# Kernel optimization log

Hardware: AMD Instinct MI355X
Metric: run time of the kernel (lower is better)

Reference implementation:

```python
import jax, jax.numpy as jnp
import numpy as np
from jax import lax

EPS_COS = 1e-8  # torch F.cosine_similarity eps
EPS_GN = 1e-5   # torch GroupNorm eps


def setup_inputs() -> dict:
    key = jax.random.key(0)
    k1, k2, k3 = jax.random.split(key, 3)
    b, f, h, w = 4, 64, 64, 64
    fdm = jax.random.uniform(k1, (b, 1, 2 * h, 2 * w), dtype=jnp.float32)
    x = jax.random.normal(k2, (b, f, h, w), dtype=jnp.float32)
    W_fuse = jax.random.normal(k3, (f, 2 * f, 3, 3), dtype=jnp.float32) * 0.05
    b_fuse = jnp.zeros((f,), jnp.float32)
    gamma = jnp.ones((f,), jnp.float32)
    beta = jnp.zeros((f,), jnp.float32)
    return {"fdm": fdm, "x": x, "W_fuse": W_fuse, "b_fuse": b_fuse,
            "gamma": gamma, "beta": beta}


def reference(fdm, x, W_fuse, b_fuse, gamma, beta):
    b, f, h, w = x.shape
    # adaptive_max_pool2d(fdm, (h, w)): input spatial is exact multiple -> plain max pool
    kh, kw = fdm.shape[2] // h, fdm.shape[3] // w
    fdm_p = lax.reduce_window(fdm, -jnp.inf, lax.max,
                              (1, 1, kh, kw), (1, 1, kh, kw), 'VALID')  # [b,1,h,w]
    # per-sample threshold: min(0.5, max(fdm)/3)
    maxv = jnp.max(fdm_p, axis=(1, 2, 3))                 # [b]
    thre = jnp.minimum(0.5, maxv / 3.0)                   # [b]
    mask = fdm_p.reshape(b, h * w) >= thre[:, None]       # [b, HW] selected pixels

    # cosine similarity between selected feature vectors and all positions.
    # Original masked-selects N rows then computes N x HW sims and max-reduces over N;
    # we compute the full HW x HW sim and mask unselected rows to -inf (same max).
    xf = x.reshape(b, f, h * w).transpose(0, 2, 1)        # [b, HW, f]
    norm = jnp.sqrt(jnp.sum(xf * xf, axis=-1, keepdims=True))
    xn = xf / jnp.maximum(norm, EPS_COS)
    sim = jnp.einsum('bpf,bqf->bpq', xn, xn)              # [b, HW(sel), HW(all)]
    sim = jnp.where(mask[:, :, None], sim, -jnp.inf)
    sm = (jnp.max(sim, axis=1) / 2.0 + 0.5).reshape(b, 1, h, w)

    # fuse: Conv2d(2f -> f, k3, pad1) + GroupNorm(1, f) + ReLU
    cat = jnp.concatenate([sm * x, x], axis=1)            # [b, 2f, h, w]
    y = lax.conv_general_dilated(cat, W_fuse, (1, 1), 'SAME',
                                 dimension_numbers=('NCHW', 'OIHW', 'NCHW'))
    y = y + b_fuse[None, :, None, None]
    mu = jnp.mean(y, axis=(1, 2, 3), keepdims=True)
    var = jnp.mean((y - mu) ** 2, axis=(1, 2, 3), keepdims=True)
    y = (y - mu) / jnp.sqrt(var + EPS_GN)
    y = y * gamma[None, :, None, None] + beta[None, :, None, None]
    x0 = jax.nn.relu(y)
    return x0, sm
```

## Files before the change

kernel.cpp:

```cpp
#include <hip/hip_runtime.h>
#include <math.h>


#define HW 4096
#define NCH 64

typedef __attribute__((ext_vector_type(8))) short short8;
typedef __attribute__((ext_vector_type(4))) float f32x4;

static __device__ __forceinline__ ushort f2bf(float f) {
    unsigned u = __float_as_uint(f);
    unsigned r = (u + 0x7fffu + ((u >> 16) & 1u)) >> 16;
    return (ushort)r;
}
static __device__ __forceinline__ float bf2f(ushort h) {
    return __uint_as_float(((unsigned)h) << 16);
}
static __device__ __forceinline__ unsigned mapf(float f) {
    unsigned u = __float_as_uint(f);
    return u ^ ((unsigned)((int)u >> 31) | 0x80000000u);
}
static __device__ __forceinline__ float unmapf(unsigned u) {
    unsigned b = (u & 0x80000000u) ? (u ^ 0x80000000u) : ~u;
    return __uint_as_float(b);
}

__global__ __launch_bounds__(256) void k_pnp(
    const float* __restrict__ fdm, const float* __restrict__ x, const float* __restrict__ W,
    float* __restrict__ pooledOut, float* __restrict__ threOut,
    int* __restrict__ unsel, int* __restrict__ unselN, unsigned* __restrict__ scores,
    float* __restrict__ gnS1, float* __restrict__ gnS2,
    float* __restrict__ rn, float* __restrict__ smOut, ushort* __restrict__ inb,
    ushort* __restrict__ wbh, ushort* __restrict__ wbl) {
    const int t = threadIdx.x;
    if (blockIdx.x < 4) {
        const int b = blockIdx.x;
        __shared__ float pooled[4096];
        __shared__ float red[256];
        __shared__ int cnt;
        const float* fb = fdm + b * 16384;
        float lmax = -1.0f;
#pragma unroll
        for (int it = 0; it < 8; ++it) {
            int id2 = it * 256 + t;
            int i = id2 >> 5;
            int j2 = id2 & 31;
            const float* base = fb + i * 256 + j2 * 4;
            float4 a = *(const float4*)base;
            float4 c = *(const float4*)(base + 128);
            float p0 = fmaxf(fmaxf(a.x, a.y), fmaxf(c.x, c.y));
            float p1 = fmaxf(fmaxf(a.z, a.w), fmaxf(c.z, c.w));
            pooled[i * 64 + j2 * 2]     = p0;
            pooled[i * 64 + j2 * 2 + 1] = p1;
            lmax = fmaxf(lmax, fmaxf(p0, p1));
        }
        red[t] = lmax;
        __syncthreads();
        for (int s = 128; s > 0; s >>= 1) {
            if (t < s) red[t] = fmaxf(red[t], red[t + s]);
            __syncthreads();
        }
        __shared__ float thre_s;
        if (t == 0) {
            thre_s = fminf(0.5f, red[0] / 3.0f);
            cnt = 0;
            gnS1[b] = 0.0f; gnS2[b] = 0.0f;
        }
        __syncthreads();
        const float th = thre_s;
#pragma unroll
        for (int it = 0; it < 4; ++it) {
            int idx = (it * 256 + t) * 4;
            *(float4*)(pooledOut + b * 4096 + idx) = *(const float4*)(pooled + idx);
        }
        for (int idx = t; idx < 4096; idx += 256) {
            scores[b * 4096 + idx] = 0u;
            if (!(pooled[idx] >= th)) {
                int pos = atomicAdd(&cnt, 1);
                unsel[b * 4096 + pos] = idx;
            }
        }
        __syncthreads();
        if (t == 0) { unselN[b] = cnt; threOut[b] = th; }
    } else if (blockIdx.x < 260) {
        __shared__ float s_part[4][64];
        const int n = blockIdx.x - 4;
        const int b = n >> 6;
        const int pbase = (n & 63) * 64;
        const int wv = t >> 6;
        const int l = t & 63;
        const int sp = pbase + l;
        const float* xp = x + b * (NCH * HW) + sp;
        float xv[16];
        float ss = 0.f;
#pragma unroll
        for (int i = 0; i < 16; ++i) {
            float a = xp[(wv * 16 + i) * HW];
            xv[i] = a;
            ss += a * a;
        }
        s_part[wv][l] = ss;
        ushort h[16];
#pragma unroll
        for (int i = 0; i < 16; ++i) h[i] = f2bf(xv[i]);
        size_t dst1 = ((size_t)(b * 8 + wv) * 4096 + sp) * 16;
        size_t dst2 = ((size_t)(b * 8 + 4 + wv) * 4096 + sp) * 16;
        *(uint4*)(inb + dst1)     = *(const uint4*)h;
        *(uint4*)(inb + dst1 + 8) = *(const uint4*)(h + 8);
        *(uint4*)(inb + dst2)     = *(const uint4*)h;
        *(uint4*)(inb + dst2 + 8) = *(const uint4*)(h + 8);
        __syncthreads();
        if (t < 64) {
            float s = s_part[0][l] + s_part[1][l] + s_part[2][l] + s_part[3][l];
            int g = b * HW + pbase + l;
            rn[g] = 1.0f / fmaxf(sqrtf(s), 1e-8f);
            smOut[g] = 1.0f;
        }
    } else {
        const int u = (blockIdx.x - 260) * 256 + t;
        const int tap = u >> 10;
        const int rem = u & 1023;
        const int oc = rem >> 4;
        const int g = rem & 15;
        ushort hh[8], ll[8];
#pragma unroll
        for (int j = 0; j < 8; ++j) {
            int ic = g * 8 + j;
            float v = W[(oc * 128 + ic) * 9 + tap];
            ushort hb = f2bf(v);
            hh[j] = hb;
            ll[j] = f2bf(v - bf2f(hb));
        }
        *(uint4*)(wbh + (size_t)u * 8) = *(const uint4*)hh;
        *(uint4*)(wbl + (size_t)u * 8) = *(const uint4*)ll;
    }
}

__global__ __launch_bounds__(256) void k_score(
    const float* __restrict__ x, const float* __restrict__ rn,
    const float* __restrict__ pooledM, const float* __restrict__ threArr,
    const int* __restrict__ unsel, const int* __restrict__ unselN,
    const ushort* __restrict__ inb, unsigned* __restrict__ scores) {
    const int b = blockIdx.y;
    const int n0 = blockIdx.x * 128;
    const int t = threadIdx.x;
    const int lane = t & 63;
    const int wave = t >> 6;
    const int li = lane & 15;
    const int quad = lane >> 4;
    const int nu = unselN[b];
    if (nu == 0) return;

    __shared__ __align__(16) ushort s_qh[64 * 72];
    __shared__ __align__(16) ushort s_ql[64 * 72];
    __shared__ unsigned s_best[64];

    const float th = threArr[b];
    const int p0 = n0 + (2 * wave) * 16 + li;
    const int p1 = n0 + (2 * wave + 1) * 16 + li;
    const float rp0 = rn[b * 4096 + p0];
    const float rp1 = rn[b * 4096 + p1];
    const float ng0 = (pooledM[b * 4096 + p0] >= th) ? 0.0f : -INFINITY;
    const float ng1 = (pooledM[b * 4096 + p1] >= th) ? 0.0f : -INFINITY;

    for (int qs0 = 0; qs0 < nu; qs0 += 64) {
        __syncthreads();
        for (int idx = t; idx < 4096; idx += 256) {
            int q_l = idx >> 6;
            int c = idx & 63;
            int qg = qs0 + q_l;
            float v = 0.0f;
            if (qg < nu) {
                int q = unsel[b * 4096 + qg];
                v = x[b * (NCH * HW) + c * HW + q] * rn[b * 4096 + q];
            }
            ushort hb = f2bf(v);
            s_qh[q_l * 72 + c] = hb;
            s_ql[q_l * 72 + c] = f2bf(v - bf2f(hb));
        }
        if (t < 64) s_best[t] = 0u;
        __syncthreads();

        f32x4 acc[2][4];
#pragma unroll
        for (int nt = 0; nt < 2; ++nt)
#pragma unroll
            for (int mt = 0; mt < 4; ++mt) acc[nt][mt] = (f32x4){0.f, 0.f, 0.f, 0.f};
#pragma unroll
        for (int k0 = 0; k0 < 2; ++k0) {
            const int cb = k0 * 32 + quad * 8;
            const int grp = 4 + (cb >> 4);
            const int sub = cb & 15;
            short8 b0 = *(const short8*)(inb + (((size_t)(b * 8 + grp) * 4096) + p0) * 16 + sub);
            short8 b1 = *(const short8*)(inb + (((size_t)(b * 8 + grp) * 4096) + p1) * 16 + sub);
#pragma unroll
            for (int mt = 0; mt < 4; ++mt) {
                short8 ah = *(const short8*)(s_qh + (size_t)(mt * 16 + li) * 72 + cb);
                short8 al = *(const short8*)(s_ql + (size_t)(mt * 16 + li) * 72 + cb);
                acc[0][mt] = __builtin_amdgcn_mfma_f32_16x16x32_bf16(ah, b0, acc[0][mt], 0, 0, 0);
                acc[0][mt] = __builtin_amdgcn_mfma_f32_16x16x32_bf16(al, b0, acc[0][mt], 0, 0, 0);
                acc[1][mt] = __builtin_amdgcn_mfma_f32_16x16x32_bf16(ah, b1, acc[1][mt], 0, 0, 0);
                acc[1][mt] = __builtin_amdgcn_mfma_f32_16x16x32_bf16(al, b1, acc[1][mt], 0, 0, 0);
            }
        }
#pragma unroll
        for (int mt = 0; mt < 4; ++mt) {
#pragma unroll
            for (int r = 0; r < 4; ++r) {
                float sc = fmaxf(acc[0][mt][r] * rp0 + ng0, acc[1][mt][r] * rp1 + ng1);
                sc = fmaxf(sc, __shfl_xor(sc, 1));
                sc = fmaxf(sc, __shfl_xor(sc, 2));
                sc = fmaxf(sc, __shfl_xor(sc, 4));
                sc = fmaxf(sc, __shfl_xor(sc, 8));
                if (li == 0) atomicMax(&s_best[mt * 16 + quad * 4 + r], mapf(sc));
            }
        }
        __syncthreads();
        if (t < 64 && qs0 + t < nu) atomicMax(scores + b * 4096 + qs0 + t, s_best[t]);
    }
}

__global__ __launch_bounds__(256) void k_conv_mfma(
    const ushort* __restrict__ inb, const ushort* __restrict__ wbh, const ushort* __restrict__ wbl,
    const float* __restrict__ bfuse, const int* __restrict__ unsel, const int* __restrict__ unselN,
    const unsigned* __restrict__ scores, float* __restrict__ smOut,
    float* __restrict__ y, float* __restrict__ gnS1, float* __restrict__ gnS2) {
    const int rowblk = blockIdx.x;
    const int ocblk = blockIdx.y;
    const int b = blockIdx.z;
    const int t = threadIdx.x;
    const int lane = t & 63;
    const int wave = t >> 6;
    const int li = lane & 15;
    const int quad = lane >> 4;
    const int h0 = rowblk * 4;
    const int oc0 = ocblk * 16;
    const int nu = unselN[b];

    __shared__ __align__(16) ushort s_in[6 * 66 * 40];
    __shared__ __align__(16) ushort s_wh[9 * 16 * 40];
    __shared__ __align__(16) ushort s_wl[9 * 16 * 40];
    __shared__ float red1[256];
    __shared__ float red2[256];

    if (rowblk == 0 && ocblk == 0) {
        for (int qi = t; qi < nu; qi += 256) {
            float sm = unmapf(scores[b * 4096 + qi]) * 0.5f + 0.5f;
            smOut[b * 4096 + unsel[b * 4096 + qi]] = sm;
        }
    }

    f32x4 acc[4];
#pragma unroll
    for (int j = 0; j < 4; ++j) acc[j] = (f32x4){0.f, 0.f, 0.f, 0.f};

    for (int chunk = 0; chunk < 4; ++chunk) {
        __syncthreads();
        for (int idx = t; idx < 1584; idx += 256) {
            int part = idx & 3;
            int cell = idx >> 2;
            int r = cell / 66;
            int c = cell - r * 66;
            int h = h0 + r - 1;
            int w = c - 1;
            uint4 v = make_uint4(0u, 0u, 0u, 0u);
            if ((unsigned)h < 64u && (unsigned)w < 64u) {
                int grp = 2 * chunk + (part >> 1);
                int sub = part & 1;
                v = *(const uint4*)(inb + (((size_t)(b * 8 + grp) * 4096 + h * 64 + w) * 16 + sub * 8));
            }
            *(uint4*)(s_in + (size_t)cell * 40 + part * 8) = v;
        }
        const int ic0 = chunk * 32;
        for (int idx = t; idx < 1152; idx += 256) {
            int part = idx & 3;
            int uu = idx >> 2;
            int hl = uu / 144;
            int rem = uu - hl * 144;
            int tap = rem >> 4;
            int o = rem & 15;
            const ushort* src = (hl ? wbl : wbh) + ((size_t)(tap * 64 + oc0 + o) * 128 + ic0 + part * 8);
            uint4 v = *(const uint4*)src;
            ushort* dst = (hl ? s_wl : s_wh) + ((size_t)(tap * 16 + o) * 40 + part * 8);
            *(uint4*)dst = v;
        }
        if (chunk < 2) {
            __syncthreads();
            for (int idx = t; idx < nu * 4; idx += 256) {
                int qi = idx >> 2;
                int part = idx & 3;
                int q = unsel[b * 4096 + qi];
                int hq = q >> 6, wq = q & 63;
                int r = hq - h0 + 1;
                if ((unsigned)r < 6u) {
                    float sm = unmapf(scores[b * 4096 + qi]) * 0.5f + 0.5f;
                    ushort* ptr = s_in + (size_t)(r * 66 + wq + 1) * 40 + part * 8;
                    ushort hv[8];
                    *(uint4*)hv = *(const uint4*)ptr;
#pragma unroll
                    for (int j = 0; j < 8; ++j) hv[j] = f2bf(bf2f(hv[j]) * sm);
                    *(uint4*)ptr = *(const uint4*)hv;
                }
            }
        }
        __syncthreads();
#pragma unroll
        for (int kh = 0; kh < 3; ++kh) {
            const int r = wave + kh;
#pragma unroll
            for (int kw = 0; kw < 3; ++kw) {
                const int tap = kh * 3 + kw;
                short8 ah = *(const short8*)(s_wh + (size_t)(tap * 16 + li) * 40 + quad * 8);
                short8 al = *(const short8*)(s_wl + (size_t)(tap * 16 + li) * 40 + quad * 8);
#pragma unroll
                for (int j = 0; j < 4; ++j) {
                    int c = j * 16 + li + kw;
                    short8 bv = *(const short8*)(s_in + ((size_t)(r * 66 + c) * 40 + quad * 8));
                    acc[j] = __builtin_amdgcn_mfma_f32_16x16x32_bf16(ah, bv, acc[j], 0, 0, 0);
                    acc[j] = __builtin_amdgcn_mfma_f32_16x16x32_bf16(al, bv, acc[j], 0, 0, 0);
                }
            }
        }
    }
    float bias[4];
#pragma unroll
    for (int reg = 0; reg < 4; ++reg) bias[reg] = bfuse[oc0 + quad * 4 + reg];
    float s1 = 0.f, s2 = 0.f;
    const int hrow = h0 + wave;
#pragma unroll
    for (int j = 0; j < 4; ++j) {
#pragma unroll
        for (int reg = 0; reg < 4; ++reg) {
            float v = acc[j][reg] + bias[reg];
            y[((size_t)(b * 64 + oc0 + quad * 4 + reg)) * HW + hrow * 64 + j * 16 + li] = v;
            s1 += v; s2 += v * v;
        }
    }
    red1[t] = s1; red2[t] = s2;
    __syncthreads();
    for (int s = 128; s > 0; s >>= 1) {
        if (t < s) { red1[t] += red1[t + s]; red2[t] += red2[t + s]; }
        __syncthreads();
    }
    if (t == 0) {
        atomicAdd(&gnS1[b], red1[0]);
        atomicAdd(&gnS2[b], red2[0]);
    }
}

__global__ void k_gn(float* __restrict__ out, const float* __restrict__ gnS1, const float* __restrict__ gnS2,
                     const float* __restrict__ gamma, const float* __restrict__ beta) {
    const int e = (blockIdx.x * 256 + threadIdx.x) * 4;
    const int b = e >> 18;
    const int c = (e >> 12) & 63;
    const float inv = 1.0f / 262144.0f;
    float mu = gnS1[b] * inv;
    float var = gnS2[b] * inv - mu * mu;
    float rs = rsqrtf(var + 1e-5f);
    float scale = rs * gamma[c];
    float shift = beta[c] - mu * scale;
    float4 v = *(const float4*)(out + e);
    float4 o;
    o.x = fmaxf(v.x * scale + shift, 0.0f);
    o.y = fmaxf(v.y * scale + shift, 0.0f);
    o.z = fmaxf(v.z * scale + shift, 0.0f);
    o.w = fmaxf(v.w * scale + shift, 0.0f);
    *(float4*)(out + e) = o;
}

extern "C" void kernel_launch(void* const* d_in, const int* in_sizes, int n_in,
                              void* d_out, int out_size, void* d_ws, size_t ws_size,
                              hipStream_t stream) {
    const float* fdm   = (const float*)d_in[0];
    const float* x     = (const float*)d_in[1];
    const float* Wf    = (const float*)d_in[2];
    const float* bfuse = (const float*)d_in[3];
    const float* gamma = (const float*)d_in[4];
    const float* beta  = (const float*)d_in[5];
    float* out = (float*)d_out;
    float* ws  = (float*)d_ws;

    float*    rn      = ws;
    float*    pooledM = rn + 16384;
    int*      unsel   = (int*)(pooledM + 16384);
    unsigned* scores  = (unsigned*)(unsel + 16384);
    float*    thre    = (float*)(scores + 16384);
    int*      unselN  = (int*)(thre + 4);
    float*    gnS1    = (float*)(unselN + 4);
    float*    gnS2    = gnS1 + 4;
    ushort*   wbh     = (ushort*)(gnS2 + 4);
    ushort*   wbl     = wbh + 73728;
    ushort*   inb     = wbl + 73728;

    float* yout  = out;
    float* smOut = out + 1048576;

    k_pnp<<<dim3(296), dim3(256), 0, stream>>>(fdm, x, Wf, pooledM, thre, unsel, unselN,
                                               scores, gnS1, gnS2, rn, smOut, inb, wbh, wbl);
    k_score<<<dim3(32, 4), dim3(256), 0, stream>>>(x, rn, pooledM, thre, unsel, unselN, inb, scores);
    k_conv_mfma<<<dim3(16, 4, 4), dim3(256), 0, stream>>>(inb, wbh, wbl, bfuse, unsel, unselN,
                                                          scores, smOut, yout, gnS1, gnS2);
    k_gn<<<dim3(1024), dim3(256), 0, stream>>>(yout, gnS1, gnS2, gamma, beta);
}
```

Before: 114.4 us.

## Store bf16 input once, gather scores from it, prefetch conv chunks in registers

Measured after the change: 120.5 us. +5.3%, slower.

```diff
diff --git a/kernel.cpp b/kernel.cpp
--- a/kernel.cpp
+++ b/kernel.cpp
@@ -103,12 +103,9 @@
         ushort h[16];
 #pragma unroll
         for (int i = 0; i < 16; ++i) h[i] = f2bf(xv[i]);
-        size_t dst1 = ((size_t)(b * 8 + wv) * 4096 + sp) * 16;
-        size_t dst2 = ((size_t)(b * 8 + 4 + wv) * 4096 + sp) * 16;
-        *(uint4*)(inb + dst1)     = *(const uint4*)h;
-        *(uint4*)(inb + dst1 + 8) = *(const uint4*)(h + 8);
-        *(uint4*)(inb + dst2)     = *(const uint4*)h;
-        *(uint4*)(inb + dst2 + 8) = *(const uint4*)(h + 8);
+        size_t dst = ((size_t)(b * 4 + wv) * 4096 + sp) * 16;
+        *(uint4*)(inb + dst)     = *(const uint4*)h;
+        *(uint4*)(inb + dst + 8) = *(const uint4*)(h + 8);
         __syncthreads();
         if (t < 64) {
             float s = s_part[0][l] + s_part[1][l] + s_part[2][l] + s_part[3][l];
@@ -137,12 +134,11 @@
 }
 
 __global__ __launch_bounds__(256) void k_score(
-    const float* __restrict__ x, const float* __restrict__ rn,
-    const float* __restrict__ pooledM, const float* __restrict__ threArr,
+    const float* __restrict__ rn, const float* __restrict__ pooledM, const float* __restrict__ threArr,
     const int* __restrict__ unsel, const int* __restrict__ unselN,
     const ushort* __restrict__ inb, unsigned* __restrict__ scores) {
     const int b = blockIdx.y;
-    const int n0 = blockIdx.x * 128;
+    const int n0 = blockIdx.x * 64;
     const int t = threadIdx.x;
     const int lane = t & 63;
     const int wave = t >> 6;
@@ -156,58 +152,60 @@
     __shared__ unsigned s_best[64];
 
     const float th = threArr[b];
-    const int p0 = n0 + (2 * wave) * 16 + li;
-    const int p1 = n0 + (2 * wave + 1) * 16 + li;
+    const int p0 = n0 + wave * 16 + li;
     const float rp0 = rn[b * 4096 + p0];
-    const float rp1 = rn[b * 4096 + p1];
     const float ng0 = (pooledM[b * 4096 + p0] >= th) ? 0.0f : -INFINITY;
-    const float ng1 = (pooledM[b * 4096 + p1] >= th) ? 0.0f : -INFINITY;
 
     for (int qs0 = 0; qs0 < nu; qs0 += 64) {
         __syncthreads();
-        for (int idx = t; idx < 4096; idx += 256) {
-            int q_l = idx >> 6;
-            int c = idx & 63;
+        for (int idx = t; idx < 512; idx += 256) {
+            int q_l = idx >> 3;
+            int part = idx & 7;
             int qg = qs0 + q_l;
-            float v = 0.0f;
+            int q = 0;
+            float rq = 0.0f;
             if (qg < nu) {
-                int q = unsel[b * 4096 + qg];
-                v = x[b * (NCH * HW) + c * HW + q] * rn[b * 4096 + q];
-            }
-            ushort hb = f2bf(v);
-            s_qh[q_l * 72 + c] = hb;
-            s_ql[q_l * 72 + c] = f2bf(v - bf2f(hb));
+                q = unsel[b * 4096 + qg];
+                rq = rn[b * 4096 + q];
+            }
+            uint4 raw = *(const uint4*)(inb + (((size_t)(b * 4 + (part >> 1)) * 4096) + q) * 16 + (part & 1) * 8);
+            ushort hv[8]; *(uint4*)hv = raw;
+            ushort hh[8], ll[8];
+#pragma unroll
+            for (int j = 0; j < 8; ++j) {
+                float v = bf2f(hv[j]) * rq;
+                hh[j] = f2bf(v);
+                ll[j] = f2bf(v - bf2f(hh[j]));
+            }
+            int c0 = (part >> 1) * 16 + (part & 1) * 8;
+            *(uint4*)(s_qh + q_l * 72 + c0) = *(const uint4*)hh;
+            *(uint4*)(s_ql + q_l * 72 + c0) = *(const uint4*)ll;
         }
         if (t < 64) s_best[t] = 0u;
         __syncthreads();
 
-        f32x4 acc[2][4];
-#pragma unroll
-        for (int nt = 0; nt < 2; ++nt)
-#pragma unroll
-            for (int mt = 0; mt < 4; ++mt) acc[nt][mt] = (f32x4){0.f, 0.f, 0.f, 0.f};
+        f32x4 acc[4];
+#pragma unroll
+        for (int mt = 0; mt < 4; ++mt) acc[mt] = (f32x4){0.f, 0.f, 0.f, 0.f};
 #pragma unroll
         for (int k0 = 0; k0 < 2; ++k0) {
             const int cb = k0 * 32 + quad * 8;
-            const int grp = 4 + (cb >> 4);
+            const int grp = cb >> 4;
             const int sub = cb & 15;
-            short8 b0 = *(const short8*)(inb + (((size_t)(b * 8 + grp) * 4096) + p0) * 16 + sub);
-            short8 b1 = *(const short8*)(inb + (((size_t)(b * 8 + grp) * 4096) + p1) * 16 + sub);
+            short8 b0 = *(const short8*)(inb + (((size_t)(b * 4 + grp) * 4096) + p0) * 16 + sub);
 #pragma unroll
             for (int mt = 0; mt < 4; ++mt) {
                 short8 ah = *(const short8*)(s_qh + (size_t)(mt * 16 + li) * 72 + cb);
                 short8 al = *(const short8*)(s_ql + (size_t)(mt * 16 + li) * 72 + cb);
-                acc[0][mt] = __builtin_amdgcn_mfma_f32_16x16x32_bf16(ah, b0, acc[0][mt], 0, 0, 0);
-                acc[0][mt] = __builtin_amdgcn_mfma_f32_16x16x32_bf16(al, b0, acc[0][mt], 0, 0, 0);
-                acc[1][mt] = __builtin_amdgcn_mfma_f32_16x16x32_bf16(ah, b1, acc[1][mt], 0, 0, 0);
-                acc[1][mt] = __builtin_amdgcn_mfma_f32_16x16x32_bf16(al, b1, acc[1][mt], 0, 0, 0);
+                acc[mt] = __builtin_amdgcn_mfma_f32_16x16x32_bf16(ah, b0, acc[mt], 0, 0, 0);
+                acc[mt] = __builtin_amdgcn_mfma_f32_16x16x32_bf16(al, b0, acc[mt], 0, 0, 0);
             }
         }
 #pragma unroll
         for (int mt = 0; mt < 4; ++mt) {
 #pragma unroll
             for (int r = 0; r < 4; ++r) {
-                float sc = fmaxf(acc[0][mt][r] * rp0 + ng0, acc[1][mt][r] * rp1 + ng1);
+                float sc = acc[mt][r] * rp0 + ng0;
                 sc = fmaxf(sc, __shfl_xor(sc, 1));
                 sc = fmaxf(sc, __shfl_xor(sc, 2));
                 sc = fmaxf(sc, __shfl_xor(sc, 4));
@@ -250,42 +248,80 @@
         }
     }
 
+    uint4 preI[7];
+    uint4 preW[5];
+    auto loadI = [&](int chunk) {
+#pragma unroll
+        for (int i = 0; i < 7; ++i) {
+            int idx = t + i * 256;
+            uint4 v = make_uint4(0u, 0u, 0u, 0u);
+            if (idx < 1584) {
+                int part = idx & 3;
+                int cell = idx >> 2;
+                int r = cell / 66;
+                int c = cell - r * 66;
+                int h = h0 + r - 1;
+                int w = c - 1;
+                if ((unsigned)h < 64u && (unsigned)w < 64u) {
+                    int grp = 2 * (chunk & 1) + (part >> 1);
+                    int sub = part & 1;
+                    v = *(const uint4*)(inb + (((size_t)(b * 4 + grp) * 4096 + h * 64 + w) * 16 + sub * 8));
+                }
+            }
+            preI[i] = v;
+        }
+    };
+    auto loadW = [&](int chunk) {
+        const int ic0 = chunk * 32;
+#pragma unroll
+        for (int i = 0; i < 5; ++i) {
+            int idx = t + i * 256;
+            if (idx < 1152) {
+                int part = idx & 3;
+                int uu = idx >> 2;
+                int hl = uu / 144;
+                int rem = uu - hl * 144;
+                int tap = rem >> 4;
+                int o = rem & 15;
+                preW[i] = *(const uint4*)((hl ? wbl : wbh) + ((size_t)(tap * 64 + oc0 + o) * 128 + ic0 + part * 8));
+            }
+        }
+    };
+
     f32x4 acc[4];
 #pragma unroll
     for (int j = 0; j < 4; ++j) acc[j] = (f32x4){0.f, 0.f, 0.f, 0.f};
 
+    loadI(0);
+    loadW(0);
+
     for (int chunk = 0; chunk < 4; ++chunk) {
         __syncthreads();
-        for (int idx = t; idx < 1584; idx += 256) {
-            int part = idx & 3;
-            int cell = idx >> 2;
-            int r = cell / 66;
-            int c = cell - r * 66;
-            int h = h0 + r - 1;
-            int w = c - 1;
-            uint4 v = make_uint4(0u, 0u, 0u, 0u);
-            if ((unsigned)h < 64u && (unsigned)w < 64u) {
-                int grp = 2 * chunk + (part >> 1);
-                int sub = part & 1;
-                v = *(const uint4*)(inb + (((size_t)(b * 8 + grp) * 4096 + h * 64 + w) * 16 + sub * 8));
-            }
-            *(uint4*)(s_in + (size_t)cell * 40 + part * 8) = v;
-        }
-        const int ic0 = chunk * 32;
-        for (int idx = t; idx < 1152; idx += 256) {
-            int part = idx & 3;
-            int uu = idx >> 2;
-            int hl = uu / 144;
-            int rem = uu - hl * 144;
-            int tap = rem >> 4;
-            int o = rem & 15;
-            const ushort* src = (hl ? wbl : wbh) + ((size_t)(tap * 64 + oc0 + o) * 128 + ic0 + part * 8);
-            uint4 v = *(const uint4*)src;
-            ushort* dst = (hl ? s_wl : s_wh) + ((size_t)(tap * 16 + o) * 40 + part * 8);
-            *(uint4*)dst = v;
-        }
+#pragma unroll
+        for (int i = 0; i < 7; ++i) {
+            int idx = t + i * 256;
+            if (idx < 1584) {
+                int part = idx & 3;
+                int cell = idx >> 2;
+                *(uint4*)(s_in + (size_t)cell * 40 + part * 8) = preI[i];
+            }
+        }
+#pragma unroll
+        for (int i = 0; i < 5; ++i) {
+            int idx = t + i * 256;
+            if (idx < 1152) {
+                int part = idx & 3;
+                int uu = idx >> 2;
+                int hl = uu / 144;
+                int rem = uu - hl * 144;
+                int tap = rem >> 4;
+                int o = rem & 15;
+                *(uint4*)((hl ? s_wl : s_wh) + ((size_t)(tap * 16 + o) * 40 + part * 8)) = preW[i];
+            }
+        }
+        if (chunk < 3) { loadI(chunk + 1); loadW(chunk + 1); }
+        __syncthreads();
         if (chunk < 2) {
-            __syncthreads();
             for (int idx = t; idx < nu * 4; idx += 256) {
                 int qi = idx >> 2;
                 int part = idx & 3;
@@ -302,8 +338,8 @@
                     *(uint4*)ptr = *(const uint4*)hv;
                 }
             }
-        }
-        __syncthreads();
+            __syncthreads();
+        }
 #pragma unroll
         for (int kh = 0; kh < 3; ++kh) {
             const int r = wave + kh;
@@ -397,7 +433,7 @@
 
     k_pnp<<<dim3(296), dim3(256), 0, stream>>>(fdm, x, Wf, pooledM, thre, unsel, unselN,
                                                scores, gnS1, gnS2, rn, smOut, inb, wbh, wbl);
-    k_score<<<dim3(32, 4), dim3(256), 0, stream>>>(x, rn, pooledM, thre, unsel, unselN, inb, scores);
+    k_score<<<dim3(64, 4), dim3(256), 0, stream>>>(rn, pooledM, thre, unsel, unselN, inb, scores);
     k_conv_mfma<<<dim3(16, 4, 4), dim3(256), 0, stream>>>(inb, wbh, wbl, bfuse, unsel, unselN,
                                                           scores, smOut, yout, gnS1, gnS2);
     k_gn<<<dim3(1024), dim3(256), 0, stream>>>(yout, gnS1, gnS2, gamma, beta);
```

## Move sm scaling into last score block and read conv input directly from global

Applied to the files above, without the earlier changes.

Result: slower. 127.4 us (+11.4%).

```diff
diff --git a/kernel.cpp b/kernel.cpp
--- a/kernel.cpp
+++ b/kernel.cpp
@@ -29,7 +29,7 @@
     const float* __restrict__ fdm, const float* __restrict__ x, const float* __restrict__ W,
     float* __restrict__ pooledOut, float* __restrict__ threOut,
     int* __restrict__ unsel, int* __restrict__ unselN, unsigned* __restrict__ scores,
-    float* __restrict__ gnS1, float* __restrict__ gnS2,
+    int* __restrict__ scoreDone, float* __restrict__ gnS1, float* __restrict__ gnS2,
     float* __restrict__ rn, float* __restrict__ smOut, ushort* __restrict__ inb,
     ushort* __restrict__ wbh, ushort* __restrict__ wbl) {
     const int t = threadIdx.x;
@@ -65,6 +65,7 @@
             thre_s = fminf(0.5f, red[0] / 3.0f);
             cnt = 0;
             gnS1[b] = 0.0f; gnS2[b] = 0.0f;
+            scoreDone[b] = 0;
         }
         __syncthreads();
         const float th = thre_s;
@@ -137,12 +138,12 @@
 }
 
 __global__ __launch_bounds__(256) void k_score(
-    const float* __restrict__ x, const float* __restrict__ rn,
-    const float* __restrict__ pooledM, const float* __restrict__ threArr,
+    const float* __restrict__ rn, const float* __restrict__ pooledM, const float* __restrict__ threArr,
     const int* __restrict__ unsel, const int* __restrict__ unselN,
-    const ushort* __restrict__ inb, unsigned* __restrict__ scores) {
+    ushort* __restrict__ inb, unsigned* __restrict__ scores, int* __restrict__ scoreDone,
+    float* __restrict__ smOut) {
     const int b = blockIdx.y;
-    const int n0 = blockIdx.x * 128;
+    const int n0 = blockIdx.x * 64;
     const int t = threadIdx.x;
     const int lane = t & 63;
     const int wave = t >> 6;
@@ -154,60 +155,63 @@
     __shared__ __align__(16) ushort s_qh[64 * 72];
     __shared__ __align__(16) ushort s_ql[64 * 72];
     __shared__ unsigned s_best[64];
+    __shared__ int s_last;
 
     const float th = threArr[b];
-    const int p0 = n0 + (2 * wave) * 16 + li;
-    const int p1 = n0 + (2 * wave + 1) * 16 + li;
+    const int p0 = n0 + wave * 16 + li;
     const float rp0 = rn[b * 4096 + p0];
-    const float rp1 = rn[b * 4096 + p1];
     const float ng0 = (pooledM[b * 4096 + p0] >= th) ? 0.0f : -INFINITY;
-    const float ng1 = (pooledM[b * 4096 + p1] >= th) ? 0.0f : -INFINITY;
 
     for (int qs0 = 0; qs0 < nu; qs0 += 64) {
         __syncthreads();
-        for (int idx = t; idx < 4096; idx += 256) {
-            int q_l = idx >> 6;
-            int c = idx & 63;
+        for (int idx = t; idx < 512; idx += 256) {
+            int q_l = idx >> 3;
+            int part = idx & 7;
             int qg = qs0 + q_l;
-            float v = 0.0f;
+            int q = 0;
+            float rq = 0.0f;
             if (qg < nu) {
-                int q = unsel[b * 4096 + qg];
-                v = x[b * (NCH * HW) + c * HW + q] * rn[b * 4096 + q];
-            }
-            ushort hb = f2bf(v);
-            s_qh[q_l * 72 + c] = hb;
-            s_ql[q_l * 72 + c] = f2bf(v - bf2f(hb));
+                q = unsel[b * 4096 + qg];
+                rq = rn[b * 4096 + q];
+            }
+            uint4 raw = *(const uint4*)(inb + (((size_t)(b * 8 + 4 + (part >> 1)) * 4096) + q) * 16 + (part & 1) * 8);
+            ushort hv[8]; *(uint4*)hv = raw;
+            ushort hh[8], ll[8];
+#pragma unroll
+            for (int j = 0; j < 8; ++j) {
+                float v = bf2f(hv[j]) * rq;
+                hh[j] = f2bf(v);
+                ll[j] = f2bf(v - bf2f(hh[j]));
+            }
+            int c0 = (part >> 1) * 16 + (part & 1) * 8;
+            *(uint4*)(s_qh + q_l * 72 + c0) = *(const uint4*)hh;
+            *(uint4*)(s_ql + q_l * 72 + c0) = *(const uint4*)ll;
         }
         if (t < 64) s_best[t] = 0u;
         __syncthreads();
 
-        f32x4 acc[2][4];
-#pragma unroll
-        for (int nt = 0; nt < 2; ++nt)
-#pragma unroll
-            for (int mt = 0; mt < 4; ++mt) acc[nt][mt] = (f32x4){0.f, 0.f, 0.f, 0.f};
+        f32x4 acc[4];
+#pragma unroll
+        for (int mt = 0; mt < 4; ++mt) acc[mt] = (f32x4){0.f, 0.f, 0.f, 0.f};
 #pragma unroll
         for (int k0 = 0; k0 < 2; ++k0) {
             const int cb = k0 * 32 + quad * 8;
             const int grp = 4 + (cb >> 4);
             const int sub = cb & 15;
             short8 b0 = *(const short8*)(inb + (((size_t)(b * 8 + grp) * 4096) + p0) * 16 + sub);
-            short8 b1 = *(const short8*)(inb + (((size_t)(b * 8 + grp) * 4096) + p1) * 16 + sub);
 #pragma unroll
             for (int mt = 0; mt < 4; ++mt) {
                 short8 ah = *(const short8*)(s_qh + (size_t)(mt * 16 + li) * 72 + cb);
                 short8 al = *(const short8*)(s_ql + (size_t)(mt * 16 + li) * 72 + cb);
-                acc[0][mt] = __builtin_amdgcn_mfma_f32_16x16x32_bf16(ah, b0, acc[0][mt], 0, 0, 0);
-                acc[0][mt] = __builtin_amdgcn_mfma_f32_16x16x32_bf16(al, b0, acc[0][mt], 0, 0, 0);
-                acc[1][mt] = __builtin_amdgcn_mfma_f32_16x16x32_bf16(ah, b1, acc[1][mt], 0, 0, 0);
-                acc[1][mt] = __builtin_amdgcn_mfma_f32_16x16x32_bf16(al, b1, acc[1][mt], 0, 0, 0);
+                acc[mt] = __builtin_amdgcn_mfma_f32_16x16x32_bf16(ah, b0, acc[mt], 0, 0, 0);
+                acc[mt] = __builtin_amdgcn_mfma_f32_16x16x32_bf16(al, b0, acc[mt], 0, 0, 0);
             }
         }
 #pragma unroll
         for (int mt = 0; mt < 4; ++mt) {
 #pragma unroll
             for (int r = 0; r < 4; ++r) {
-                float sc = fmaxf(acc[0][mt][r] * rp0 + ng0, acc[1][mt][r] * rp1 + ng1);
+                float sc = acc[mt][r] * rp0 + ng0;
                 sc = fmaxf(sc, __shfl_xor(sc, 1));
                 sc = fmaxf(sc, __shfl_xor(sc, 2));
                 sc = fmaxf(sc, __shfl_xor(sc, 4));
@@ -218,13 +222,33 @@
         __syncthreads();
         if (t < 64 && qs0 + t < nu) atomicMax(scores + b * 4096 + qs0 + t, s_best[t]);
     }
+    __threadfence();
+    if (t == 0) s_last = (atomicAdd(&scoreDone[b], 1) == 63);
+    __syncthreads();
+    if (s_last) {
+        for (int idx = t; idx < nu * 4; idx += 256) {
+            int qi = idx >> 2;
+            int part = idx & 3;
+            int q = unsel[b * 4096 + qi];
+            float sm = unmapf(atomicOr(&scores[b * 4096 + qi], 0u)) * 0.5f + 0.5f;
+            if (part == 0) smOut[b * 4096 + q] = sm;
+            const ushort* src = inb + ((size_t)(b * 8 + 4 + part) * 4096 + q) * 16;
+            ushort* dst = inb + ((size_t)(b * 8 + part) * 4096 + q) * 16;
+            ushort hv[16];
+            *(uint4*)hv       = *(const uint4*)src;
+            *(uint4*)(hv + 8) = *(const uint4*)(src + 8);
+#pragma unroll
+            for (int j = 0; j < 16; ++j) hv[j] = f2bf(bf2f(hv[j]) * sm);
+            *(uint4*)dst       = *(const uint4*)hv;
+            *(uint4*)(dst + 8) = *(const uint4*)(hv + 8);
+        }
+    }
 }
 
 __global__ __launch_bounds__(256) void k_conv_mfma(
     const ushort* __restrict__ inb, const ushort* __restrict__ wbh, const ushort* __restrict__ wbl,
-    const float* __restrict__ bfuse, const int* __restrict__ unsel, const int* __restrict__ unselN,
-    const unsigned* __restrict__ scores, float* __restrict__ smOut,
-    float* __restrict__ y, float* __restrict__ gnS1, float* __restrict__ gnS2) {
+    const float* __restrict__ bfuse, float* __restrict__ y,
+    float* __restrict__ gnS1, float* __restrict__ gnS2) {
     const int rowblk = blockIdx.x;
     const int ocblk = blockIdx.y;
     const int b = blockIdx.z;
@@ -233,44 +257,22 @@
     const int wave = t >> 6;
     const int li = lane & 15;
     const int quad = lane >> 4;
-    const int h0 = rowblk * 4;
     const int oc0 = ocblk * 16;
-    const int nu = unselN[b];
-
-    __shared__ __align__(16) ushort s_in[6 * 66 * 40];
+    const int hr = rowblk * 2 + (wave >> 1);
+    const int j0 = (wave & 1) * 2;
+
     __shared__ __align__(16) ushort s_wh[9 * 16 * 40];
     __shared__ __align__(16) ushort s_wl[9 * 16 * 40];
     __shared__ float red1[256];
     __shared__ float red2[256];
 
-    if (rowblk == 0 && ocblk == 0) {
-        for (int qi = t; qi < nu; qi += 256) {
-            float sm = unmapf(scores[b * 4096 + qi]) * 0.5f + 0.5f;
-            smOut[b * 4096 + unsel[b * 4096 + qi]] = sm;
-        }
-    }
-
-    f32x4 acc[4];
-#pragma unroll
-    for (int j = 0; j < 4; ++j) acc[j] = (f32x4){0.f, 0.f, 0.f, 0.f};
+    const short8 zero8 = (short8){0, 0, 0, 0, 0, 0, 0, 0};
+    f32x4 acc[2];
+    acc[0] = (f32x4){0.f, 0.f, 0.f, 0.f};
+    acc[1] = (f32x4){0.f, 0.f, 0.f, 0.f};
 
     for (int chunk = 0; chunk < 4; ++chunk) {
         __syncthreads();
-        for (int idx = t; idx < 1584; idx += 256) {
-            int part = idx & 3;
-            int cell = idx >> 2;
-            int r = cell / 66;
-            int c = cell - r * 66;
-            int h = h0 + r - 1;
-            int w = c - 1;
-            uint4 v = make_uint4(0u, 0u, 0u, 0u);
-            if ((unsigned)h < 64u && (unsigned)w < 64u) {
-                int grp = 2 * chunk + (part >> 1);
-                int sub = part & 1;
-                v = *(const uint4*)(inb + (((size_t)(b * 8 + grp) * 4096 + h * 64 + w) * 16 + sub * 8));
-            }
-            *(uint4*)(s_in + (size_t)cell * 40 + part * 8) = v;
-        }
         const int ic0 = chunk * 32;
         for (int idx = t; idx < 1152; idx += 256) {
             int part = idx & 3;
@@ -279,60 +281,41 @@
             int rem = uu - hl * 144;
             int tap = rem >> 4;
             int o = rem & 15;
-            const ushort* src = (hl ? wbl : wbh) + ((size_t)(tap * 64 + oc0 + o) * 128 + ic0 + part * 8);
-            uint4 v = *(const uint4*)src;
-            ushort* dst = (hl ? s_wl : s_wh) + ((size_t)(tap * 16 + o) * 40 + part * 8);
-            *(uint4*)dst = v;
-        }
-        if (chunk < 2) {
-            __syncthreads();
-            for (int idx = t; idx < nu * 4; idx += 256) {
-                int qi = idx >> 2;
-                int part = idx & 3;
-                int q = unsel[b * 4096 + qi];
-                int hq = q >> 6, wq = q & 63;
-                int r = hq - h0 + 1;
-                if ((unsigned)r < 6u) {
-                    float sm = unmapf(scores[b * 4096 + qi]) * 0.5f + 0.5f;
-                    ushort* ptr = s_in + (size_t)(r * 66 + wq + 1) * 40 + part * 8;
-                    ushort hv[8];
-                    *(uint4*)hv = *(const uint4*)ptr;
-#pragma unroll
-                    for (int j = 0; j < 8; ++j) hv[j] = f2bf(bf2f(hv[j]) * sm);
-                    *(uint4*)ptr = *(const uint4*)hv;
-                }
-            }
-        }
-        __syncthreads();
+            uint4 v = *(const uint4*)((hl ? wbl : wbh) + ((size_t)(tap * 64 + oc0 + o) * 128 + ic0 + part * 8));
+            *(uint4*)((hl ? s_wl : s_wh) + ((size_t)(tap * 16 + o) * 40 + part * 8)) = v;
+        }
+        __syncthreads();
+        const ushort* bbase = inb + ((size_t)(b * 8 + 2 * chunk + (quad >> 1)) * 4096) * 16 + (quad & 1) * 8;
 #pragma unroll
         for (int kh = 0; kh < 3; ++kh) {
-            const int r = wave + kh;
+            const int r = hr + kh - 1;
+            const bool rok = (unsigned)r < 64u;
+            const int rbase = (rok ? r : 0) * 64;
 #pragma unroll
             for (int kw = 0; kw < 3; ++kw) {
                 const int tap = kh * 3 + kw;
                 short8 ah = *(const short8*)(s_wh + (size_t)(tap * 16 + li) * 40 + quad * 8);
                 short8 al = *(const short8*)(s_wl + (size_t)(tap * 16 + li) * 40 + quad * 8);
 #pragma unroll
-                for (int j = 0; j < 4; ++j) {
-                    int c = j * 16 + li + kw;
-                    short8 bv = *(const short8*)(s_in + ((size_t)(r * 66 + c) * 40 + quad * 8));
-                    acc[j] = __builtin_amdgcn_mfma_f32_16x16x32_bf16(ah, bv, acc[j], 0, 0, 0);
-                    acc[j] = __builtin_amdgcn_mfma_f32_16x16x32_bf16(al, bv, acc[j], 0, 0, 0);
+                for (int jj = 0; jj < 2; ++jj) {
+                    const int w = (j0 + jj) * 16 + li + kw - 1;
+                    const bool ok = rok && ((unsigned)w < 64u);
+                    const int sp = rbase + (ok ? w : 0);
+                    short8 bv = *(const short8*)(bbase + (size_t)sp * 16);
+                    bv = ok ? bv : zero8;
+                    acc[jj] = __builtin_amdgcn_mfma_f32_16x16x32_bf16(ah, bv, acc[jj], 0, 0, 0);
+                    acc[jj] = __builtin_amdgcn_mfma_f32_16x16x32_bf16(al, bv, acc[jj], 0, 0, 0);
                 }
             }
         }
     }
-    float bias[4];
-#pragma unroll
-    for (int reg = 0; reg < 4; ++reg) bias[reg] = bfuse[oc0 + quad * 4 + reg];
     float s1 = 0.f, s2 = 0.f;
-    const int hrow = h0 + wave;
-#pragma unroll
-    for (int j = 0; j < 4; ++j) {
+#pragma unroll
+    for (int jj = 0; jj < 2; ++jj) {
 #pragma unroll
         for (int reg = 0; reg < 4; ++reg) {
-            float v = acc[j][reg] + bias[reg];
-            y[((size_t)(b * 64 + oc0 + quad * 4 + reg)) * HW + hrow * 64 + j * 16 + li] = v;
+            float v = acc[jj][reg] + bfuse[oc0 + quad * 4 + reg];
+            y[((size_t)(b * 64 + oc0 + quad * 4 + reg)) * HW + hr * 64 + (j0 + jj) * 16 + li] = v;
             s1 += v; s2 += v * v;
         }
     }
@@ -380,25 +363,26 @@
     float* out = (float*)d_out;
     float* ws  = (float*)d_ws;
 
-    float*    rn      = ws;
-    float*    pooledM = rn + 16384;
-    int*      unsel   = (int*)(pooledM + 16384);
-    unsigned* scores  = (unsigned*)(unsel + 16384);
-    float*    thre    = (float*)(scores + 16384);
-    int*      unselN  = (int*)(thre + 4);
-    float*    gnS1    = (float*)(unselN + 4);
-    float*    gnS2    = gnS1 + 4;
-    ushort*   wbh     = (ushort*)(gnS2 + 4);
-    ushort*   wbl     = wbh + 73728;
-    ushort*   inb     = wbl + 73728;
+    float*    rn       = ws;
+    float*    pooledM  = rn + 16384;
+    int*      unsel    = (int*)(pooledM + 16384);
+    unsigned* scores   = (unsigned*)(unsel + 16384);
+    float*    thre     = (float*)(scores + 16384);
+    int*      unselN   = (int*)(thre + 4);
+    float*    gnS1     = (float*)(unselN + 4);
+    float*    gnS2     = gnS1 + 4;
+    int*      scoreDone= (int*)(gnS2 + 4);
+    ushort*   wbh      = (ushort*)(scoreDone + 4);
+    ushort*   wbl      = wbh + 73728;
+    ushort*   inb      = wbl + 73728;
 
     float* yout  = out;
     float* smOut = out + 1048576;
 
     k_pnp<<<dim3(296), dim3(256), 0, stream>>>(fdm, x, Wf, pooledM, thre, unsel, unselN,
-                                               scores, gnS1, gnS2, rn, smOut, inb, wbh, wbl);
-    k_score<<<dim3(32, 4), dim3(256), 0, stream>>>(x, rn, pooledM, thre, unsel, unselN, inb, scores);
-    k_conv_mfma<<<dim3(16, 4, 4), dim3(256), 0, stream>>>(inb, wbh, wbl, bfuse, unsel, unselN,
-                                                          scores, smOut, yout, gnS1, gnS2);
+                                               scores, scoreDone, gnS1, gnS2, rn, smOut, inb, wbh, wbl);
+    k_score<<<dim3(64, 4), dim3(256), 0, stream>>>(rn, pooledM, thre, unsel, unselN,
+                                                   inb, scores, scoreDone, smOut);
+    k_conv_mfma<<<dim3(32, 4, 4), dim3(256), 0, stream>>>(inb, wbh, wbl, bfuse, yout, gnS1, gnS2);
     k_gn<<<dim3(1024), dim3(256), 0, stream>>>(yout, gnS1, gnS2, gamma, beta);
 }
```
